# Performance work log

Hardware: AMD Instinct MI355X
Metric: run time of the kernel (lower is better)

The kernel has to match this reference:

```python
import jax, jax.numpy as jnp
from jax import lax
import numpy as np

VOCAB, TAGS, EMBED, HIDDEN, BATCH, SEQ = 50000, 9, 300, 1000, 32, 200


def setup_inputs() -> dict:
    key = jax.random.key(0)
    ks = jax.random.split(key, 12)
    s_e = 1.0 / np.sqrt(HIDDEN)
    inp = {
        "x": jax.random.randint(ks[0], (SEQ, BATCH), 0, VOCAB),
        "y": jax.random.randint(ks[1], (SEQ, BATCH), 0, TAGS),
        "embed_w": jax.random.normal(ks[2], (VOCAB, EMBED), jnp.float32),
        "W_ih": jax.random.uniform(ks[3], (4 * HIDDEN, EMBED), jnp.float32, -s_e, s_e),
        "W_hh": jax.random.uniform(ks[4], (4 * HIDDEN, HIDDEN), jnp.float32, -s_e, s_e),
        "b_ih": jax.random.uniform(ks[5], (4 * HIDDEN,), jnp.float32, -s_e, s_e),
        "b_hh": jax.random.uniform(ks[6], (4 * HIDDEN,), jnp.float32, -s_e, s_e),
        "lin_w": jax.random.uniform(ks[7], (TAGS, HIDDEN), jnp.float32, -s_e, s_e),
        "lin_b": jax.random.uniform(ks[8], (TAGS,), jnp.float32, -s_e, s_e),
        "start_trans": jax.random.uniform(ks[9], (TAGS,), jnp.float32, -0.1, 0.1),
        "end_trans": jax.random.uniform(ks[10], (TAGS,), jnp.float32, -0.1, 0.1),
        "trans": jax.random.uniform(ks[11], (TAGS, TAGS), jnp.float32, -0.1, 0.1),
    }
    return inp


def _forward(x, y, embed_w, W_ih, W_hh, b_ih, b_hh, lin_w, lin_b, start_trans, end_trans, trans):
    T, B = x.shape
    H = W_hh.shape[1]
    embeds = embed_w[x]  # [T,B,E]
    # Precompute input contribution to gates: [T,B,4H]
    xg = jnp.einsum("tbe,ge->tbg", embeds, W_ih) + b_ih + b_hh

    def lstm_step(carry, xg_t):
        h, c = carry
        g = xg_t + h @ W_hh.T  # [B,4H]
        i, f, gg, o = jnp.split(g, 4, axis=-1)  # PyTorch gate order i,f,g,o
        c = jax.nn.sigmoid(f) * c + jax.nn.sigmoid(i) * jnp.tanh(gg)
        h = jax.nn.sigmoid(o) * jnp.tanh(c)
        return (h, c), h

    h0 = jnp.zeros((B, H), embeds.dtype)
    _, hs = lax.scan(lstm_step, (h0, h0), xg)  # hs: [T,B,H]

    tag_space = jnp.einsum("tbh,kh->tbk", hs, lin_w) + lin_b  # [T,B,K]
    # Faithful to original: log_softmax over dim=1 (the batch axis)
    emissions = jax.nn.log_softmax(tag_space, axis=1)

    # ---- CRF log-likelihood (pytorch-crf semantics, full mask, sum reduction) ----
    b_idx = jnp.arange(B)
    em_at_y = jnp.take_along_axis(emissions, y[:, :, None], axis=2)[:, :, 0]  # [T,B]
    numerator = (
        start_trans[y[0]]
        + em_at_y.sum(axis=0)
        + trans[y[:-1], y[1:]].sum(axis=0)
        + end_trans[y[-1]]
    )  # [B]

    alpha0 = start_trans[None, :] + emissions[0]  # [B,K]

    def crf_step(alpha, em_t):
        # alpha: [B,K] over previous tag; em_t: [B,K]
        nxt = jax.nn.logsumexp(alpha[:, :, None] + trans[None, :, :] + em_t[:, None, :], axis=1)
        return nxt, None

    alpha, _ = lax.scan(crf_step, alpha0, emissions[1:])
    log_z = jax.nn.logsumexp(alpha + end_trans[None, :], axis=1)  # [B]
    return (numerator - log_z).sum()


def reference(x, y, embed_w, W_ih, W_hh, b_ih, b_hh, lin_w, lin_b, start_trans, end_trans, trans):
    return _forward(x, y, embed_w, W_ih, W_hh, b_ih, b_hh, lin_w, lin_b, start_trans, end_trans, trans)
```

## Files before the change

### kernel.cpp

```cpp
#include <hip/hip_runtime.h>

#define T_SEQ 200
#define NB    32
#define NE    300
#define NH    1000
#define NK    9
#define NJ    4096
#define EPD   320
#define WSCALE 256.0f
#define HSCALE 16.0f
#define LSCALE 512.0f
#define GSCALE (1.0f / (256.0f * 16.0f))
#define TSCALE (1.0f / (16.0f * 512.0f))

typedef __attribute__((ext_vector_type(4))) float f32x4;
typedef __attribute__((ext_vector_type(8))) short s16x8;
typedef __attribute__((ext_vector_type(4))) short s16x4;
typedef unsigned long long u64;

__device__ __forceinline__ unsigned short f2bf(float f) {
    union { float f; unsigned u; } v; v.f = f;
    unsigned r = v.u + 0x7FFFu + ((v.u >> 16) & 1u);
    return (unsigned short)(r >> 16);
}
__device__ __forceinline__ float bf2f(unsigned short h) {
    union { unsigned u; float f; } v; v.u = ((unsigned)h) << 16;
    return v.f;
}
__device__ __forceinline__ float ftanh(float x) {
    float e = __expf(fminf(2.f * x, 80.f));
    return (e - 1.f) / (e + 1.f);
}
__device__ __forceinline__ float fsig(float x) {
    return 1.f / (1.f + __expf(-x));
}
__device__ __forceinline__ unsigned nt_poll(const unsigned* p) {
    unsigned r;
    asm volatile("global_load_dword %0, %1, off nt\n\t"
                 "s_waitcnt vmcnt(0)"
                 : "=v"(r) : "v"(p) : "memory");
    return r;
}
__device__ __forceinline__ void plain_pub(unsigned* p, unsigned v) {
    __hip_atomic_store(p, v, __ATOMIC_RELAXED, __HIP_MEMORY_SCOPE_WORKGROUP);
}

__global__ __launch_bounds__(256) void prep_emb(
    const int* __restrict__ x, const float* __restrict__ embed_w,
    unsigned short* __restrict__ emb_bf, unsigned* __restrict__ ctrl)
{
    const int t = blockIdx.x, tid = threadIdx.x;
    if (blockIdx.x == 0) {
        for (int i = tid; i < 2048; i += 256)
            ctrl[i] = (i == 497) ? 0xffffffffu : 0u;
    }
    for (int idx = tid; idx < NB * EPD; idx += 256) {
        int b = idx / EPD, e = idx - b * EPD;
        float v = (e < NE) ? embed_w[(size_t)x[t * NB + b] * NE + e] : 0.f;
        emb_bf[((size_t)t * NB + b) * EPD + e] = f2bf(v);
    }
}

__global__ __launch_bounds__(256) void prep_w(
    const float* __restrict__ W_ih, const float* __restrict__ b_ih,
    const float* __restrict__ b_hh, const float* __restrict__ lin_w,
    unsigned short* __restrict__ wih_bf, float* __restrict__ biasg,
    unsigned char* __restrict__ linw_q)
{
    const int blk = blockIdx.x, tid = threadIdx.x;
    for (int idx = tid; idx < 64 * EPD; idx += 256) {
        int jr = idx / EPD, e = idx - jr * EPD;
        int jp = blk * 64 + jr;
        int wgu = jp >> 7, rr = jp & 127, g = rr >> 5, uu = rr & 31;
        int m = wgu * 32 + uu;
        float v = (m < NH && e < NE) ? W_ih[(size_t)(g * NH + m) * NE + e] : 0.f;
        wih_bf[(size_t)jp * EPD + e] = f2bf(v);
    }
    if (tid < 64) {
        int jp = blk * 64 + tid;
        int wgu = jp >> 7, rr = jp & 127, g = rr >> 5, uu = rr & 31;
        int m = wgu * 32 + uu;
        biasg[jp] = (m < NH) ? (b_ih[g * NH + m] + b_hh[g * NH + m]) : 0.f;
    }
    if (blk < 16) {
        int n = blk, k = tid * 4;
        float v0 = (n < NK && k + 0 < NH) ? lin_w[(size_t)n * NH + k + 0] * LSCALE : 0.f;
        float v1 = (n < NK && k + 1 < NH) ? lin_w[(size_t)n * NH + k + 1] * LSCALE : 0.f;
        float v2 = (n < NK && k + 2 < NH) ? lin_w[(size_t)n * NH + k + 2] * LSCALE : 0.f;
        float v3 = (n < NK && k + 3 < NH) ? lin_w[(size_t)n * NH + k + 3] * LSCALE : 0.f;
        int p01 = __builtin_amdgcn_cvt_pk_fp8_f32(v0, v1, 0, false);
        int p23 = __builtin_amdgcn_cvt_pk_fp8_f32(v2, v3, 0, false);
        ((unsigned*)linw_q)[n * 256 + tid] =
            ((unsigned)p01 & 0xffffu) | ((unsigned)p23 << 16);
    }
}

__device__ __forceinline__ int gate_xg(unsigned* done, int ready, int tn, int lane) {
    while (ready <= tn) {
        unsigned v = 64u;
        if (lane < 8 && ready + lane < T_SEQ)
            v = __hip_atomic_load(&done[ready + lane], __ATOMIC_RELAXED,
                                  __HIP_MEMORY_SCOPE_AGENT);
        unsigned m = (unsigned)__ballot((int)(v >= 64u)) & 255u;
        if (m & 1u) {
            unsigned run = (m == 255u) ? 8u : (unsigned)__builtin_ctz(~m);
            ready += (int)run;
        } else {
            __builtin_amdgcn_s_sleep(1);
        }
    }
    return ready;
}

__global__ __launch_bounds__(256, 1) void lstm_kernel(
    const float* __restrict__ W_hh,
    const unsigned short* __restrict__ emb_bf,
    const unsigned short* __restrict__ wih_bf,
    const float* __restrict__ biasg,
    unsigned short* __restrict__ xg,
    unsigned char* __restrict__ h_q,
    unsigned* __restrict__ ctrl)
{
    __shared__ __align__(16) unsigned char s_w[128 * 1024];
    __shared__ int s_chunk, s_grp, s_pid, s_mode;

    const int tid = threadIdx.x;

    if (tid == 0) {
        unsigned xcc;
        asm volatile("s_getreg_b32 %0, hwreg(HW_REG_XCC_ID)" : "=s"(xcc));
        xcc &= 15u;
        unsigned myidx = __hip_atomic_fetch_add(&ctrl[480 + xcc], 1u,
                             __ATOMIC_RELAXED, __HIP_MEMORY_SCOPE_AGENT);
        __threadfence();
        unsigned tot = __hip_atomic_fetch_add(&ctrl[496], 1u,
                             __ATOMIC_RELAXED, __HIP_MEMORY_SCOPE_AGENT);
        if (tot == 255u) {
            __threadfence();
            unsigned w0 = 0xffu, w1 = 0xffu;
            for (unsigned xx = 0; xx < 16; ++xx) {
                unsigned cx = __hip_atomic_load(&ctrl[480 + xx], __ATOMIC_RELAXED,
                                                __HIP_MEMORY_SCOPE_AGENT);
                if (cx >= 32u) {
                    if (w0 == 0xffu) w0 = xx;
                    else { w1 = xx; break; }
                }
            }
            __hip_atomic_store(&ctrl[497], w0 | (w1 << 8), __ATOMIC_RELAXED,
                               __HIP_MEMORY_SCOPE_AGENT);
        }
        unsigned win;
        do {
            win = __hip_atomic_load(&ctrl[497], __ATOMIC_RELAXED,
                                    __HIP_MEMORY_SCOPE_AGENT);
        } while (win == 0xffffffffu);
        unsigned w0 = win & 0xffu, w1 = (win >> 8) & 0xffu;
        int grp = -1;
        if (xcc == w0 && myidx < 32u) grp = 0;
        else if (xcc == w1 && myidx < 32u) grp = 1;
        s_grp = grp;
        s_chunk = (grp >= 0) ? (int)myidx : -1;
        s_pid = (grp >= 0) ? -1
                     : (int)__hip_atomic_fetch_add(&ctrl[498], 1u,
                           __ATOMIC_RELAXED, __HIP_MEMORY_SCOPE_AGENT);
    }
    __syncthreads();
    const int chunk = s_chunk;
    const int w = tid >> 6, lane = tid & 63;
    const int col = lane & 15, quad = lane >> 4;
    unsigned* done = ctrl + 256;

    if (chunk < 0) {
        const int pid = s_pid;
        for (int g = pid; g < T_SEQ * 64; g += 192) {
            const int t = g >> 6, jt = g & 63;
            const unsigned short* eb = emb_bf + (size_t)t * NB * EPD;
            const unsigned short* wb = wih_bf + (size_t)(jt * 64 + w * 16 + col) * EPD;
            const unsigned short* ea0 = eb + (size_t)col * EPD;
            const unsigned short* ea1 = eb + (size_t)(16 + col) * EPD;

            f32x4 acc0 = {0.f, 0.f, 0.f, 0.f};
            f32x4 acc1 = {0.f, 0.f, 0.f, 0.f};
#pragma unroll
            for (int kc = 0; kc < EPD / 32; ++kc) {
                int ko = kc * 32 + quad * 8;
                s16x8 a0 = *(const s16x8*)&ea0[ko];
                s16x8 a1 = *(const s16x8*)&ea1[ko];
                s16x8 bb = *(const s16x8*)&wb[ko];
                acc0 = __builtin_amdgcn_mfma_f32_16x16x32_bf16(a0, bb, acc0, 0, 0, 0);
                acc1 = __builtin_amdgcn_mfma_f32_16x16x32_bf16(a1, bb, acc1, 0, 0, 0);
            }
            const int jp = jt * 64 + w * 16 + col;
            const float bi = biasg[jp];
            size_t base = ((size_t)t * NJ + jp) * NB;
            union { s16x4 v; u64 q; } p0, p1;
#pragma unroll
            for (int r = 0; r < 4; ++r) {
                p0.v[r] = (short)f2bf(acc0[r] + bi);
                p1.v[r] = (short)f2bf(acc1[r] + bi);
            }
            __hip_atomic_store((u64*)&xg[base + quad * 4], p0.q,
                               __ATOMIC_RELAXED, __HIP_MEMORY_SCOPE_AGENT);
            __hip_atomic_store((u64*)&xg[base + 16 + quad * 4], p1.q,
                               __ATOMIC_RELAXED, __HIP_MEMORY_SCOPE_AGENT);
            __syncthreads();
            if (tid == 0)
                __hip_atomic_fetch_add(&done[t], 1u, __ATOMIC_RELAXED,
                                       __HIP_MEMORY_SCOPE_AGENT);
        }
        return;
    }

    const int grp = s_grp;
    const size_t GOFF = (size_t)grp * 16384;
    unsigned* slowf = ctrl + grp * 64;
    unsigned* fastf = ctrl + 128 + grp * 64;
    unsigned* s_w32 = (unsigned*)s_w;

    for (int idx = tid; idx < 128 * 256; idx += 256) {
        int r = idx >> 8, dw = idx & 255;
        int g = r >> 5, uu = r & 31, m = chunk * 32 + uu;
        float4 w4 = make_float4(0.f, 0.f, 0.f, 0.f);
        if (m < NH && dw < 250)
            w4 = *(const float4*)&W_hh[(size_t)(g * NH + m) * NH + dw * 4];
        int p0 = __builtin_amdgcn_cvt_pk_fp8_f32(w4.x * WSCALE, w4.y * WSCALE, 0, false);
        int p1 = __builtin_amdgcn_cvt_pk_fp8_f32(w4.z * WSCALE, w4.w * WSCALE, 0, false);
        unsigned v = ((unsigned)p0 & 0xffffu) | ((unsigned)p1 << 16);
        int kb = dw >> 1;
        int kbs = kb ^ (r & 15);
        s_w32[r * 256 + (kbs << 1) + (dw & 1)] = v;
    }
    if (tid < 128)
        *(unsigned*)(h_q + GOFF + (size_t)chunk * 512 + tid * 4) = 0u;
    __syncthreads();
    if (tid == 0) {
        plain_pub(&fastf[chunk * 2 + 0], 1u);
        plain_pub(&fastf[chunk * 2 + 1], 1u);
        __hip_atomic_store(&slowf[chunk * 2 + 0], 1u, __ATOMIC_RELAXED,
                           __HIP_MEMORY_SCOPE_AGENT);
        __hip_atomic_store(&slowf[chunk * 2 + 1], 1u, __ATOMIC_RELAXED,
                           __HIP_MEMORY_SCOPE_AGENT);
    }
    if (grp == 0 && chunk == 0 && w == 0) {
        int md = 2;
        for (int it = 0; it < 8192; ++it) {
            unsigned v = nt_poll(&fastf[lane]);
            if (__all((int)(v >= 1u))) { md = 1; break; }
        }
        if (lane == 0) {
            __hip_atomic_store(&ctrl[499], (unsigned)md, __ATOMIC_RELAXED,
                               __HIP_MEMORY_SCOPE_AGENT);
            s_mode = md;
        }
    } else if (tid == 0) {
        unsigned m;
        do {
            m = __hip_atomic_load(&ctrl[499], __ATOMIC_RELAXED,
                                  __HIP_MEMORY_SCOPE_AGENT);
        } while (m == 0u);
        s_mode = (int)m;
    }
    __syncthreads();
    const int mode = s_mode;

    if (w >= 2) return;
    const int p = w;
    const int fid = chunk * 2 + w;

    int ready = gate_xg(done, 0, 1, lane);
    s16x4 xcur[4], xnxt[4];
#pragma unroll
    for (int g = 0; g < 4; ++g)
        xcur[g] = *(const s16x4*)&xg[((size_t)0 * NJ + chunk * 128 + (2 * g + p) * 16 + col) * NB
                                     + grp * 16 + quad * 4];

    float c[4] = {0.f, 0.f, 0.f, 0.f};
    const int rw = quad * 4;
    const int boff = col * 32 + quad * 8;

    for (int t = 0; t < T_SEQ; ++t) {
        const unsigned need = (unsigned)(t + 1);
        const int gt = t + 2;
        bool gate_pending = (gt < T_SEQ) && (ready <= gt);
        if (mode == 1) {
            for (;;) {
                unsigned v = nt_poll(&fastf[lane]);
                bool hok = __all((int)(v >= need));
                if (gate_pending) {
                    unsigned d = 64u;
                    if (lane < 8 && ready + lane < T_SEQ)
                        d = __hip_atomic_load(&done[ready + lane], __ATOMIC_RELAXED,
                                              __HIP_MEMORY_SCOPE_AGENT);
                    unsigned m = (unsigned)__ballot((int)(d >= 64u)) & 255u;
                    if (m & 1u)
                        ready += (m == 255u) ? 8 : (int)__builtin_ctz(~m);
                    gate_pending = (ready <= gt);
                }
                if (hok && !gate_pending) break;
            }
        } else {
            for (;;) {
                unsigned v = __hip_atomic_load(&slowf[lane], __ATOMIC_RELAXED,
                                               __HIP_MEMORY_SCOPE_AGENT);
                bool hok = __all((int)(v >= need));
                if (gate_pending) {
                    unsigned d = 64u;
                    if (lane < 8 && ready + lane < T_SEQ)
                        d = __hip_atomic_load(&done[ready + lane], __ATOMIC_RELAXED,
                                              __HIP_MEMORY_SCOPE_AGENT);
                    unsigned m = (unsigned)__ballot((int)(d >= 64u)) & 255u;
                    if (m & 1u)
                        ready += (m == 255u) ? 8 : (int)__builtin_ctz(~m);
                    gate_pending = (ready <= gt);
                }
                if (hok && !gate_pending) break;
            }
        }
        asm volatile("" ::: "memory");

        const unsigned char* pb = h_q + (size_t)t * 32768 + GOFF + boff;
        u64 a[32];
#pragma unroll
        for (int kc = 0; kc < 32; ++kc)
            a[kc] = *(const u64*)(pb + (size_t)kc * 512);

        if (t + 1 < T_SEQ) {
#pragma unroll
            for (int g = 0; g < 4; ++g)
                xnxt[g] = *(const s16x4*)&xg[((size_t)(t + 1) * NJ + chunk * 128 + (2 * g + p) * 16 + col) * NB
                                             + grp * 16 + quad * 4];
        }

        f32x4 acc0 = {0.f, 0.f, 0.f, 0.f};
        f32x4 acc1 = {0.f, 0.f, 0.f, 0.f};
        f32x4 acc2 = {0.f, 0.f, 0.f, 0.f};
        f32x4 acc3 = {0.f, 0.f, 0.f, 0.f};
#pragma unroll
        for (int kc = 0; kc < 32; ++kc) {
            int kb = kc * 4 + quad;
            u64 b0 = *(const u64*)&s_w[((0 * 2 + p) * 16 + col) * 1024 + ((kb ^ col) << 3)];
            u64 b1 = *(const u64*)&s_w[((1 * 2 + p) * 16 + col) * 1024 + ((kb ^ col) << 3)];
            u64 b2 = *(const u64*)&s_w[((2 * 2 + p) * 16 + col) * 1024 + ((kb ^ col) << 3)];
            u64 b3 = *(const u64*)&s_w[((3 * 2 + p) * 16 + col) * 1024 + ((kb ^ col) << 3)];
            acc0 = __builtin_amdgcn_mfma_f32_16x16x32_fp8_fp8((long)a[kc], (long)b0, acc0, 0, 0, 0);
            acc1 = __builtin_amdgcn_mfma_f32_16x16x32_fp8_fp8((long)a[kc], (long)b1, acc1, 0, 0, 0);
            acc2 = __builtin_amdgcn_mfma_f32_16x16x32_fp8_fp8((long)a[kc], (long)b2, acc2, 0, 0, 0);
            acc3 = __builtin_amdgcn_mfma_f32_16x16x32_fp8_fp8((long)a[kc], (long)b3, acc3, 0, 0, 0);
        }

        float hv[4];
#pragma unroll
        for (int r = 0; r < 4; ++r) {
            float gi = acc0[r] * GSCALE + bf2f((unsigned short)xcur[0][r]);
            float gf = acc1[r] * GSCALE + bf2f((unsigned short)xcur[1][r]);
            float gg = acc2[r] * GSCALE + bf2f((unsigned short)xcur[2][r]);
            float go = acc3[r] * GSCALE + bf2f((unsigned short)xcur[3][r]);
            c[r] = fsig(gf) * c[r] + fsig(gi) * ftanh(gg);
            hv[r] = fsig(go) * ftanh(c[r]);
        }
        {
            int p01 = __builtin_amdgcn_cvt_pk_fp8_f32(hv[0] * HSCALE, hv[1] * HSCALE, 0, false);
            int p23 = __builtin_amdgcn_cvt_pk_fp8_f32(hv[2] * HSCALE, hv[3] * HSCALE, 0, false);
            unsigned char* pg = h_q + (size_t)(t + 1) * 32768 + GOFF + (size_t)chunk * 512
                              + p * 16 + col;
            pg[(rw + 0) * 32] = (unsigned char)(p01 & 0xff);
            pg[(rw + 1) * 32] = (unsigned char)((p01 >> 8) & 0xff);
            pg[(rw + 2) * 32] = (unsigned char)(p23 & 0xff);
            pg[(rw + 3) * 32] = (unsigned char)((p23 >> 8) & 0xff);
        }
        asm volatile("s_waitcnt vmcnt(0)" ::: "memory");
        if (lane == 0) {
            plain_pub(&fastf[fid], (unsigned)(t + 2));
            if (mode == 2)
                __hip_atomic_store(&slowf[fid], (unsigned)(t + 2),
                                   __ATOMIC_RELAXED, __HIP_MEMORY_SCOPE_AGENT);
        }
#pragma unroll
        for (int g = 0; g < 4; ++g) xcur[g] = xnxt[g];
    }
}

__global__ __launch_bounds__(64) void tag_gemm(
    const unsigned char* __restrict__ h_q,
    const unsigned char* __restrict__ linw_q, float* __restrict__ ts)
{
    const int m0 = blockIdx.x * 16, lane = threadIdx.x;
    const int col = lane & 15, quad = lane >> 4;
    const int m = m0 + col, t = m >> 5, b = m & 31;
    const int g = b >> 4, bl = b & 15;
    const unsigned char* pa = h_q + (size_t)(t + 1) * 32768 + (size_t)g * 16384
                            + bl * 32 + quad * 8;
    const unsigned char* pw = linw_q + (size_t)col * 1024 + quad * 8;

    f32x4 acc = {0.f, 0.f, 0.f, 0.f};
#pragma unroll 8
    for (int kc = 0; kc < 32; ++kc) {
        u64 a  = *(const u64*)(pa + (size_t)kc * 512);
        u64 bv = *(const u64*)(pw + kc * 32);
        acc = __builtin_amdgcn_mfma_f32_16x16x32_fp8_fp8((long)a, (long)bv, acc, 0, 0, 0);
    }
#pragma unroll
    for (int r = 0; r < 4; ++r)
        ts[(size_t)(m0 + quad * 4 + r) * 16 + col] = acc[r] * TSCALE;
}

__global__ __launch_bounds__(320) void em_kernel(
    const float* __restrict__ ts, const float* __restrict__ lin_b,
    float* __restrict__ em)
{
    __shared__ float s_ts[NB * NK];
    __shared__ float s_lse[NK];
    const int t = blockIdx.x, tid = threadIdx.x;
    float val = 0.f;
    int b = tid / NK, k = tid - b * NK;
    if (tid < NB * NK) {
        val = ts[(size_t)(t * NB + b) * 16 + k] + lin_b[k];
        s_ts[b * NK + k] = val;
    }
    __syncthreads();
    if (tid < NK) {
        float m = -1e30f;
        for (int bb = 0; bb < NB; ++bb) m = fmaxf(m, s_ts[bb * NK + tid]);
        float s = 0.f;
        for (int bb = 0; bb < NB; ++bb) s += __expf(s_ts[bb * NK + tid] - m);
        s_lse[tid] = m + __logf(s);
    }
    __syncthreads();
    if (tid < NB * NK)
        em[((size_t)t * NB + b) * NK + k] = val - s_lse[k];
}

__global__ __launch_bounds__(320) void crf_kernel(
    const int* __restrict__ y, const float* __restrict__ em,
    const float* __restrict__ start_trans, const float* __restrict__ end_trans,
    const float* __restrict__ trans, float* __restrict__ out)
{
    __shared__ float s_trans[NK * NK];
    __shared__ float s_alpha[NB * NK];
    __shared__ float s_red[NB];
    const int tid = threadIdx.x;
    if (tid < NK * NK) s_trans[tid] = trans[tid];
    __syncthreads();

    float num = 0.f;
    if (tid < NB) {
        int b = tid, yp = y[b];
        num = start_trans[yp] + em[(size_t)b * NK + yp];
        for (int t = 1; t < T_SEQ; ++t) {
            int yc = y[t * NB + b];
            num += s_trans[yp * NK + yc] + em[((size_t)t * NB + b) * NK + yc];
            yp = yc;
        }
        num += end_trans[yp];
    }

    const int b = tid / NK, k = tid - (tid / NK) * NK;
    if (tid < NB * NK)
        s_alpha[tid] = start_trans[k] + em[(size_t)b * NK + k];
    __syncthreads();

    for (int t = 1; t < T_SEQ; ++t) {
        float nv = 0.f;
        if (tid < NB * NK) {
            float m = -1e30f;
#pragma unroll
            for (int i = 0; i < NK; ++i)
                m = fmaxf(m, s_alpha[b * NK + i] + s_trans[i * NK + k]);
            float s = 0.f;
#pragma unroll
            for (int i = 0; i < NK; ++i)
                s += __expf(s_alpha[b * NK + i] + s_trans[i * NK + k] - m);
            nv = em[((size_t)t * NB + b) * NK + k] + m + __logf(s);
        }
        __syncthreads();
        if (tid < NB * NK) s_alpha[tid] = nv;
        __syncthreads();
    }

    if (tid < NB) {
        float m = -1e30f;
        for (int k2 = 0; k2 < NK; ++k2)
            m = fmaxf(m, s_alpha[tid * NK + k2] + end_trans[k2]);
        float s = 0.f;
        for (int k2 = 0; k2 < NK; ++k2)
            s += __expf(s_alpha[tid * NK + k2] + end_trans[k2] - m);
        s_red[tid] = num - (m + __logf(s));
    }
    __syncthreads();
    if (tid == 0) {
        float tot = 0.f;
        for (int i = 0; i < NB; ++i) tot += s_red[i];
        out[0] = tot;
    }
}

extern "C" void kernel_launch(void* const* d_in, const int* in_sizes, int n_in,
                              void* d_out, int out_size, void* d_ws, size_t ws_size,
                              hipStream_t stream)
{
    const int*   x           = (const int*)d_in[0];
    const int*   y           = (const int*)d_in[1];
    const float* embed_w     = (const float*)d_in[2];
    const float* W_ih        = (const float*)d_in[3];
    const float* W_hh        = (const float*)d_in[4];
    const float* b_ih        = (const float*)d_in[5];
    const float* b_hh        = (const float*)d_in[6];
    const float* lin_w       = (const float*)d_in[7];
    const float* lin_b       = (const float*)d_in[8];
    const float* start_trans = (const float*)d_in[9];
    const float* end_trans   = (const float*)d_in[10];
    const float* trans       = (const float*)d_in[11];
    float* out = (float*)d_out;

    char* ws = (char*)d_ws;
    unsigned short* xg     = (unsigned short*)(ws);
    float*          ts     = (float*)(ws);
    unsigned char*  h_q    = (unsigned char*)(ws + 52428800);
    unsigned char*  linw_q = (unsigned char*)(ws + 59015168);
    float*          em     = (float*)(ws + 65601536);
    unsigned*       ctrl   = (unsigned*)(ws + 65831936);
    float*          biasg  = (float*)(ws + 65840128);
    unsigned short* emb_bf = (unsigned short*)(ws + 65856512);
    unsigned short* wih_bf = (unsigned short*)(ws + 69952512);

    prep_emb<<<dim3(T_SEQ), 256, 0, stream>>>(x, embed_w, emb_bf, ctrl);
    prep_w<<<dim3(64), 256, 0, stream>>>(W_ih, b_ih, b_hh, lin_w, wih_bf, biasg, linw_q);

    lstm_kernel<<<dim3(256), 256, 0, stream>>>(W_hh, emb_bf, wih_bf, biasg,
                                               xg, h_q, ctrl);

    tag_gemm<<<dim3(400), 64, 0, stream>>>(h_q, linw_q, ts);
    em_kernel<<<dim3(T_SEQ), 320, 0, stream>>>(ts, lin_b, em);
    crf_kernel<<<dim3(1), 320, 0, stream>>>(y, em, start_trans, end_trans, trans, out);
}
```

Before: 1.054 ms.

## Fuse tag GEMM with emission softmax and rewrite CRF scan with shuffles

Merges the tag-projection GEMM and the batch-axis log-softmax into one kernel per timestep, so the intermediate tag-space buffer and one kernel launch are gone. The CRF kernel is restructured so each batch element runs in a 16-lane group. Alpha exchange uses wave shuffles instead of shared memory plus two block barriers per step. Emissions are prefetched eight timesteps ahead and labels are staged in shared memory; the numerator is computed alongside the forward recursion. This targets the serial 199-step CRF latency chain and launch overhead, at the cost of more register use in the CRF kernel.

After: 983.5 us. 6.7% less time.

```diff
diff --git a/kernel.cpp b/kernel.cpp
--- a/kernel.cpp
+++ b/kernel.cpp
@@ -380,16 +380,19 @@
     }
 }
 
-__global__ __launch_bounds__(64) void tag_gemm(
+__global__ __launch_bounds__(128) void tagem_kernel(
     const unsigned char* __restrict__ h_q,
-    const unsigned char* __restrict__ linw_q, float* __restrict__ ts)
+    const unsigned char* __restrict__ linw_q,
+    const float* __restrict__ lin_b,
+    float* __restrict__ em)
 {
-    const int m0 = blockIdx.x * 16, lane = threadIdx.x;
+    __shared__ float s_ts[NB * NK];
+    __shared__ float s_lse[NK];
+    const int t = blockIdx.x, tid = threadIdx.x;
+    const int w = tid >> 6, lane = tid & 63;
     const int col = lane & 15, quad = lane >> 4;
-    const int m = m0 + col, t = m >> 5, b = m & 31;
-    const int g = b >> 4, bl = b & 15;
-    const unsigned char* pa = h_q + (size_t)(t + 1) * 32768 + (size_t)g * 16384
-                            + bl * 32 + quad * 8;
+    const unsigned char* pa = h_q + (size_t)(t + 1) * 32768 + (size_t)w * 16384
+                            + col * 32 + quad * 8;
     const unsigned char* pw = linw_q + (size_t)col * 1024 + quad * 8;
 
     f32x4 acc = {0.f, 0.f, 0.f, 0.f};
@@ -399,23 +402,11 @@
         u64 bv = *(const u64*)(pw + kc * 32);
         acc = __builtin_amdgcn_mfma_f32_16x16x32_fp8_fp8((long)a, (long)bv, acc, 0, 0, 0);
     }
-#pragma unroll
-    for (int r = 0; r < 4; ++r)
-        ts[(size_t)(m0 + quad * 4 + r) * 16 + col] = acc[r] * TSCALE;
-}
-
-__global__ __launch_bounds__(320) void em_kernel(
-    const float* __restrict__ ts, const float* __restrict__ lin_b,
-    float* __restrict__ em)
-{
-    __shared__ float s_ts[NB * NK];
-    __shared__ float s_lse[NK];
-    const int t = blockIdx.x, tid = threadIdx.x;
-    float val = 0.f;
-    int b = tid / NK, k = tid - b * NK;
-    if (tid < NB * NK) {
-        val = ts[(size_t)(t * NB + b) * 16 + k] + lin_b[k];
-        s_ts[b * NK + k] = val;
+    if (col < NK) {
+        float lb = lin_b[col];
+#pragma unroll
+        for (int r = 0; r < 4; ++r)
+            s_ts[(w * 16 + quad * 4 + r) * NK + col] = acc[r] * TSCALE + lb;
     }
     __syncthreads();
     if (tid < NK) {
@@ -426,66 +417,91 @@
         s_lse[tid] = m + __logf(s);
     }
     __syncthreads();
-    if (tid < NB * NK)
-        em[((size_t)t * NB + b) * NK + k] = val - s_lse[k];
-}
-
-__global__ __launch_bounds__(320) void crf_kernel(
+    for (int idx = tid; idx < NB * NK; idx += 128) {
+        int k = idx - (idx / NK) * NK;
+        em[(size_t)t * NB * NK + idx] = s_ts[idx] - s_lse[k];
+    }
+}
+
+__global__ __launch_bounds__(512) void crf_kernel(
     const int* __restrict__ y, const float* __restrict__ em,
     const float* __restrict__ start_trans, const float* __restrict__ end_trans,
     const float* __restrict__ trans, float* __restrict__ out)
 {
     __shared__ float s_trans[NK * NK];
-    __shared__ float s_alpha[NB * NK];
     __shared__ float s_red[NB];
+    __shared__ int   s_y[T_SEQ * NB];
     const int tid = threadIdx.x;
+    const int gb = tid >> 4;
+    const int q  = tid & 15;
+    const int lane = tid & 63;
+    const int gbase = lane & 48;
+
     if (tid < NK * NK) s_trans[tid] = trans[tid];
-    __syncthreads();
-
-    float num = 0.f;
-    if (tid < NB) {
-        int b = tid, yp = y[b];
-        num = start_trans[yp] + em[(size_t)b * NK + yp];
-        for (int t = 1; t < T_SEQ; ++t) {
-            int yc = y[t * NB + b];
-            num += s_trans[yp * NK + yc] + em[((size_t)t * NB + b) * NK + yc];
-            yp = yc;
-        }
-        num += end_trans[yp];
-    }
-
-    const int b = tid / NK, k = tid - (tid / NK) * NK;
-    if (tid < NB * NK)
-        s_alpha[tid] = start_trans[k] + em[(size_t)b * NK + k];
-    __syncthreads();
-
-    for (int t = 1; t < T_SEQ; ++t) {
-        float nv = 0.f;
-        if (tid < NB * NK) {
-            float m = -1e30f;
-#pragma unroll
-            for (int i = 0; i < NK; ++i)
-                m = fmaxf(m, s_alpha[b * NK + i] + s_trans[i * NK + k]);
-            float s = 0.f;
-#pragma unroll
-            for (int i = 0; i < NK; ++i)
-                s += __expf(s_alpha[b * NK + i] + s_trans[i * NK + k] - m);
-            nv = em[((size_t)t * NB + b) * NK + k] + m + __logf(s);
-        }
-        __syncthreads();
-        if (tid < NB * NK) s_alpha[tid] = nv;
-        __syncthreads();
-    }
-
-    if (tid < NB) {
-        float m = -1e30f;
-        for (int k2 = 0; k2 < NK; ++k2)
-            m = fmaxf(m, s_alpha[tid * NK + k2] + end_trans[k2]);
-        float s = 0.f;
-        for (int k2 = 0; k2 < NK; ++k2)
-            s += __expf(s_alpha[tid * NK + k2] + end_trans[k2] - m);
-        s_red[tid] = num - (m + __logf(s));
-    }
+    for (int i = tid; i < T_SEQ * NB; i += 512) s_y[i] = y[i];
+    __syncthreads();
+
+    float trC[NK];
+#pragma unroll
+    for (int i = 0; i < NK; ++i)
+        trC[i] = (q < NK) ? s_trans[i * NK + q] : 0.f;
+
+    float emv0 = (q < NK) ? em[gb * NK + q] : -1e30f;
+    int yp = s_y[gb];
+    float num = start_trans[yp] + __shfl(emv0, gbase | yp, 64);
+    float alpha = (q < NK) ? (start_trans[q] + emv0) : -1e30f;
+
+    float e[8];
+#pragma unroll
+    for (int j = 0; j < 8; ++j) {
+        int t = 1 + j;
+        e[j] = (q < NK && t < T_SEQ) ? em[(size_t)(t * NB + gb) * NK + q] : -1e30f;
+    }
+    for (int blk = 0; blk < 25; ++blk) {
+        float enx[8];
+        const int tb = 1 + (blk + 1) * 8;
+#pragma unroll
+        for (int j = 0; j < 8; ++j) {
+            int t = tb + j;
+            enx[j] = (q < NK && t < T_SEQ) ? em[(size_t)(t * NB + gb) * NK + q] : -1e30f;
+        }
+#pragma unroll
+        for (int j = 0; j < 8; ++j) {
+            int t = 1 + blk * 8 + j;
+            if (t < T_SEQ) {
+                float ev = e[j];
+                int yc = s_y[t * NB + gb];
+                num += s_trans[yp * NK + yc] + __shfl(ev, gbase | yc, 64);
+                yp = yc;
+                float a_i[NK];
+#pragma unroll
+                for (int i = 0; i < NK; ++i)
+                    a_i[i] = __shfl(alpha, gbase | i, 64) + trC[i];
+                float m = a_i[0];
+#pragma unroll
+                for (int i = 1; i < NK; ++i) m = fmaxf(m, a_i[i]);
+                float s = 0.f;
+#pragma unroll
+                for (int i = 0; i < NK; ++i) s += __expf(a_i[i] - m);
+                alpha = (q < NK) ? (ev + m + __logf(s)) : -1e30f;
+            }
+        }
+#pragma unroll
+        for (int j = 0; j < 8; ++j) e[j] = enx[j];
+    }
+
+    num += end_trans[yp];
+    float v = (q < NK) ? (alpha + end_trans[q]) : -1e30f;
+    float mg = v;
+#pragma unroll
+    for (int off = 8; off >= 1; off >>= 1)
+        mg = fmaxf(mg, __shfl_xor(mg, off, 64));
+    float sg = __expf(v - mg);
+#pragma unroll
+    for (int off = 8; off >= 1; off >>= 1)
+        sg += __shfl_xor(sg, off, 64);
+    float lz = mg + __logf(sg);
+    if (q == 0) s_red[gb] = num - lz;
     __syncthreads();
     if (tid == 0) {
         float tot = 0.f;
@@ -514,7 +530,6 @@
 
     char* ws = (char*)d_ws;
     unsigned short* xg     = (unsigned short*)(ws);
-    float*          ts     = (float*)(ws);
     unsigned char*  h_q    = (unsigned char*)(ws + 52428800);
     unsigned char*  linw_q = (unsigned char*)(ws + 59015168);
     float*          em     = (float*)(ws + 65601536);
@@ -529,7 +544,6 @@
     lstm_kernel<<<dim3(256), 256, 0, stream>>>(W_hh, emb_bf, wih_bf, biasg,
                                                xg, h_q, ctrl);
 
-    tag_gemm<<<dim3(400), 64, 0, stream>>>(h_q, linw_q, ts);
-    em_kernel<<<dim3(T_SEQ), 320, 0, stream>>>(ts, lin_b, em);
-    crf_kernel<<<dim3(1), 320, 0, stream>>>(y, em, start_trans, end_trans, trans, out);
-}
+    tagem_kernel<<<dim3(T_SEQ), 128, 0, stream>>>(h_q, linw_q, lin_b, em);
+    crf_kernel<<<dim3(1), 512, 0, stream>>>(y, em, start_trans, end_trans, trans, out);
+}
```
